# Optimization experiments

Hardware: AMD Instinct MI355X
Metric: run time of the kernel (lower is better)

Reference implementation:

```python
import jax, jax.numpy as jnp
import numpy as np
import math

B, C, H, W = 8, 64, 256, 256
E, NH = 256, 8
HD = E // NH  # 32


def get_coords(h, w):
    xx, yy = jnp.meshgrid(jnp.arange(h, dtype=jnp.float32), jnp.arange(w, dtype=jnp.float32), indexing='ij')
    return jnp.stack((xx.reshape(-1), yy.reshape(-1)), axis=-1)  # [N, 2]


def setup_inputs() -> dict:
    key = jax.random.key(0)
    ks = jax.random.split(key, 12)
    def xavier(k, shape):
        fan_out, fan_in = shape
        a = math.sqrt(6.0 / (fan_in + fan_out))
        return jax.random.uniform(k, shape, jnp.float32, -a, a)
    x = jax.random.normal(ks[0], (B, C, H, W), jnp.float32)
    z = jax.random.normal(ks[1], (B, C), jnp.float32)
    pos = jax.random.uniform(ks[2], (B, NH, 2), jnp.float32) * (H - 1)
    Wq = xavier(ks[3], (E, C)); bq = jnp.zeros((E,), jnp.float32)
    Wk = xavier(ks[4], (E, C)); bk = jnp.zeros((E,), jnp.float32)
    Wv = xavier(ks[5], (E, C)); bv = jnp.zeros((E,), jnp.float32)
    Wp = xavier(ks[6], (HD, 2)); bp = jax.random.uniform(ks[7], (HD,), jnp.float32, -1.0, 1.0) / math.sqrt(2.0)
    return {"x": x, "z": z, "pos": pos, "Wq": Wq, "bq": bq, "Wk": Wk, "bk": bk,
            "Wv": Wv, "bv": bv, "Wp": Wp, "bp": bp}


def reference(x, z, pos, Wq, bq, Wk, bk, Wv, bv, Wp, bp):
    b, c, h, w = x.shape
    n = h * w
    x_flat = x.reshape(b, c, n).transpose(0, 2, 1)          # [B, N, C]
    pos_grid = get_coords(h, w)                              # [N, 2]
    q = (z @ Wq.T + bq).reshape(b, NH, HD)                   # [B, H, hd]
    k = (x_flat @ Wk.T + bk).reshape(b, n, NH, HD)           # [B, N, H, hd]
    # relative-position modulation of keys
    rel = pos_grid[None, :, None, :] - pos[:, None, :, :]    # [B, N, H, 2]
    qxk = rel @ Wp.T + bp                                    # [B, N, H, hd]
    k = k * qxk
    v = x_flat @ Wv.T + bv                                   # [B, N, E]
    attn_logits = jnp.einsum('bhc,bnhc->bnh', q, k) / math.sqrt(HD)
    attention = jax.nn.softmax(attn_logits, axis=1)          # softmax over N
    pos_out = jnp.einsum('bnh,nx->bhx', attention, pos_grid) # [B, H, 2]
    values = jnp.einsum('bnh,bnc->bhc', attention, v)        # [B, H, E]
    return (values, pos_out)
```

## Files before the change

kernel.cpp:

```cpp
#include <hip/hip_runtime.h>

#define NN    65536
#define NSUB  256
#define NBLK  (NN/NSUB)
#define WPAD  260

#define OFF_W   0
#define SZ_W    (8*64*24)
#define OFF_CJ  (OFF_W + SZ_W)
#define SZ_CJ   (8*24)
#define OFF_PM  (OFF_CJ + SZ_CJ)
#define SZ_P    (8*NBLK*8)
#define OFF_PL  (OFF_PM + SZ_P)
#define OFF_PSP (OFF_PL + SZ_P)
#define OFF_PSX (OFF_PSP + 2*SZ_P)

#define SMEM1_FLOATS (64*WPAD + 8*NSUB + 128)
#define SMEM1_BYTES  (SMEM1_FLOATS*4)

__global__ __launch_bounds__(64) void prep_kernel(
    const float* __restrict__ z,  const float* __restrict__ Wq, const float* __restrict__ bq,
    const float* __restrict__ Wk, const float* __restrict__ bk,
    const float* __restrict__ Wp, const float* __restrict__ bp,
    float* __restrict__ Weff, float* __restrict__ Cj)
{
  const int h = blockIdx.x, b = blockIdx.y, t = threadIdx.x;
  __shared__ float q[32];
  if (t < 32) {
    const int e = h*32 + t;
    float a = bq[e];
    const float* zr = z + b*64;
    const float* wr = Wq + e*64;
    #pragma unroll 8
    for (int c = 0; c < 64; ++c) a += zr[c]*wr[c];
    q[t] = a;
  }
  __syncthreads();
  {
    const int c = t;
    float w0 = 0.f, w1 = 0.f, w2 = 0.f;
    #pragma unroll 4
    for (int hd = 0; hd < 32; ++hd) {
      const float qk = q[hd] * Wk[(h*32+hd)*64 + c];
      w0 += qk * bp[hd];
      w1 += qk * Wp[hd*2+0];
      w2 += qk * Wp[hd*2+1];
    }
    float* o = Weff + (b*64 + c)*24 + h*3;
    o[0] = w0; o[1] = w1; o[2] = w2;
  }
  if (t < 3) {
    float s = 0.f;
    for (int hd = 0; hd < 32; ++hd) {
      const float m = (t == 0) ? bp[hd] : Wp[hd*2 + (t-1)];
      s += q[hd] * m * bk[h*32+hd];
    }
    Cj[b*24 + h*3 + t] = s;
  }
}

__global__ __launch_bounds__(256) void main_kernel(
    const float* __restrict__ x, const float* __restrict__ pos,
    const float* __restrict__ Weff, const float* __restrict__ Cj,
    float* __restrict__ Pm, float* __restrict__ Pl,
    float* __restrict__ Psp, float* __restrict__ Psx)
{
  extern __shared__ float sm[];
  float* xs  = sm;
  float* ps  = sm + 64*WPAD;
  float* red = ps + 8*NSUB;
  const int t   = threadIdx.x;
  const int blk = blockIdx.x;
  const int b   = blockIdx.y;
  const int n0  = blk * NSUB;

  {
    const float* xb = x + (size_t)b*64*NN + n0;
    #pragma unroll
    for (int r = 0; r < 16; ++r) {
      const int f  = t + r*256;
      const int c  = f >> 6;
      const int p4 = (f & 63) << 2;
      const float4 v = *(const float4*)(xb + (size_t)c*NN + p4);
      *(float4*)(xs + c*WPAD + p4) = v;
    }
  }

  float cj[24];
  #pragma unroll
  for (int k = 0; k < 24; ++k) cj[k] = Cj[b*24 + k];
  float px[8], py[8];
  #pragma unroll
  for (int h = 0; h < 8; ++h) { px[h] = pos[(b*8+h)*2 + 0]; py[h] = pos[(b*8+h)*2 + 1]; }

  __syncthreads();

  float acc[24];
  #pragma unroll
  for (int k = 0; k < 24; ++k) acc[k] = cj[k];
  const float* wb = Weff + b*64*24;
  for (int c = 0; c < 64; ++c) {
    const float xv = xs[c*WPAD + t];
    const float* wr = wb + c*24;
    #pragma unroll
    for (int k = 0; k < 24; ++k) acc[k] += wr[k]*xv;
  }
  const int   n  = n0 + t;
  const float gx = (float)(n >> 8);
  const float gy = (float)(n & 255);
  float lg[8];
  #pragma unroll
  for (int h = 0; h < 8; ++h) {
    const float rx = gx - px[h];
    const float ry = gy - py[h];
    lg[h] = (acc[h*3+0] + rx*acc[h*3+1] + ry*acc[h*3+2]) * 0.17677669529663687f;
  }

  float mh[8];
  #pragma unroll
  for (int h = 0; h < 8; ++h) {
    float m = lg[h];
    #pragma unroll
    for (int off = 32; off >= 1; off >>= 1) m = fmaxf(m, __shfl_xor(m, off, 64));
    mh[h] = m;
  }
  const int wid = t >> 6, lid = t & 63;
  if (lid == 0) {
    #pragma unroll
    for (int h = 0; h < 8; ++h) red[h*4 + wid] = mh[h];
  }
  __syncthreads();

  float p[8], trip[24];
  #pragma unroll
  for (int h = 0; h < 8; ++h) {
    const float M = fmaxf(fmaxf(red[h*4+0], red[h*4+1]), fmaxf(red[h*4+2], red[h*4+3]));
    mh[h] = M;
    p[h]  = __expf(lg[h] - M);
    trip[h*3+0] = p[h];
    trip[h*3+1] = p[h]*gx;
    trip[h*3+2] = p[h]*gy;
  }
  #pragma unroll
  for (int k = 0; k < 24; ++k) {
    float s = trip[k];
    #pragma unroll
    for (int off = 32; off >= 1; off >>= 1) s += __shfl_xor(s, off, 64);
    trip[k] = s;
  }
  if (lid == 0) {
    #pragma unroll
    for (int k = 0; k < 24; ++k) red[32 + k*4 + wid] = trip[k];
  }
  #pragma unroll
  for (int h = 0; h < 8; ++h) ps[h*NSUB + t] = p[h];
  __syncthreads();

  if (t < 8) {
    const int h = t;
    const int base = (b*NBLK + blk)*8 + h;
    Pm[base] = mh[h];
    Pl[base] = red[32+(h*3+0)*4+0] + red[32+(h*3+0)*4+1] + red[32+(h*3+0)*4+2] + red[32+(h*3+0)*4+3];
    Psp[base*2+0] = red[32+(h*3+1)*4+0] + red[32+(h*3+1)*4+1] + red[32+(h*3+1)*4+2] + red[32+(h*3+1)*4+3];
    Psp[base*2+1] = red[32+(h*3+2)*4+0] + red[32+(h*3+2)*4+1] + red[32+(h*3+2)*4+2] + red[32+(h*3+2)*4+3];
  }

  {
    const int c  = t & 63;
    const int h0 = t >> 6;
    const float* xr  = xs + c*WPAD;
    const float* pr0 = ps + h0*NSUB;
    const float* pr1 = ps + (h0+4)*NSUB;
    float a0 = 0.f, a1 = 0.f;
    #pragma unroll 4
    for (int nn = 0; nn < NSUB; nn += 4) {
      const float4 xv = *(const float4*)(xr  + nn);
      const float4 q0 = *(const float4*)(pr0 + nn);
      const float4 q1 = *(const float4*)(pr1 + nn);
      a0 += xv.x*q0.x + xv.y*q0.y + xv.z*q0.z + xv.w*q0.w;
      a1 += xv.x*q1.x + xv.y*q1.y + xv.z*q1.z + xv.w*q1.w;
    }
    const int pb = (b*NBLK + blk)*8;
    Psx[(pb + h0    )*64 + c] = a0;
    Psx[(pb + h0 + 4)*64 + c] = a1;
  }
}

__global__ __launch_bounds__(256) void finish_kernel(
    const float* __restrict__ Pm, const float* __restrict__ Pl,
    const float* __restrict__ Psp, const float* __restrict__ Psx,
    const float* __restrict__ Wv, const float* __restrict__ bv,
    float* __restrict__ out)
{
  const int h = blockIdx.x, b = blockIdx.y, t = threadIdx.x;
  __shared__ float al[256];
  __shared__ float red[16];
  __shared__ float sxl[256];
  __shared__ float SXs[64];
  const int wid = t >> 6, lid = t & 63;
  const int pbase = (b*NBLK + t)*8 + h;

  const float m_t = Pm[pbase];
  float mm = m_t;
  #pragma unroll
  for (int off = 32; off >= 1; off >>= 1) mm = fmaxf(mm, __shfl_xor(mm, off, 64));
  if (lid == 0) red[wid] = mm;
  __syncthreads();
  const float M = fmaxf(fmaxf(red[0], red[1]), fmaxf(red[2], red[3]));
  const float a = __expf(m_t - M);
  al[t] = a;
  float lt  = Pl[pbase] * a;
  float sxt = Psp[pbase*2+0] * a;
  float syt = Psp[pbase*2+1] * a;
  #pragma unroll
  for (int off = 32; off >= 1; off >>= 1) {
    lt  += __shfl_xor(lt,  off, 64);
    sxt += __shfl_xor(sxt, off, 64);
    syt += __shfl_xor(syt, off, 64);
  }
  if (lid == 0) { red[4+wid] = lt; red[8+wid] = sxt; red[12+wid] = syt; }
  __syncthreads();
  const float L = red[4]+red[5]+red[6]+red[7];
  const float invL = 1.0f / L;

  const int c = t & 63, g = t >> 6;
  float acc = 0.f;
  for (int k = 0; k < 64; ++k) {
    const int blk = g*64 + k;
    acc += Psx[((b*NBLK + blk)*8 + h)*64 + c] * al[blk];
  }
  sxl[g*64 + c] = acc;
  __syncthreads();
  if (t < 64) SXs[t] = (sxl[t] + sxl[64+t] + sxl[128+t] + sxl[192+t]) * invL;
  __syncthreads();

  float v = bv[t];
  const float* wvr = Wv + t*64;
  #pragma unroll 8
  for (int c2 = 0; c2 < 64; ++c2) v += wvr[c2] * SXs[c2];
  out[(b*8+h)*256 + t] = v;

  if (t == 0) {
    const float SPx = red[8]+red[9]+red[10]+red[11];
    const float SPy = red[12]+red[13]+red[14]+red[15];
    out[16384 + (b*8+h)*2 + 0] = SPx * invL;
    out[16384 + (b*8+h)*2 + 1] = SPy * invL;
  }
}

extern "C" void kernel_launch(void* const* d_in, const int* in_sizes, int n_in,
                              void* d_out, int out_size, void* d_ws, size_t ws_size,
                              hipStream_t stream)
{
  const float* x   = (const float*)d_in[0];
  const float* z   = (const float*)d_in[1];
  const float* pos = (const float*)d_in[2];
  const float* Wq  = (const float*)d_in[3];
  const float* bq  = (const float*)d_in[4];
  const float* Wk  = (const float*)d_in[5];
  const float* bk  = (const float*)d_in[6];
  const float* Wv  = (const float*)d_in[7];
  const float* bv  = (const float*)d_in[8];
  const float* Wp  = (const float*)d_in[9];
  const float* bp  = (const float*)d_in[10];
  float* out = (float*)d_out;
  float* ws  = (float*)d_ws;

  float* Weff = ws + OFF_W;
  float* Cj   = ws + OFF_CJ;
  float* Pm   = ws + OFF_PM;
  float* Pl   = ws + OFF_PL;
  float* Psp  = ws + OFF_PSP;
  float* Psx  = ws + OFF_PSX;

  (void)hipFuncSetAttribute((const void*)main_kernel,
                            hipFuncAttributeMaxDynamicSharedMemorySize, SMEM1_BYTES);

  prep_kernel  <<<dim3(8,8),    64,  0,           stream>>>(z, Wq, bq, Wk, bk, Wp, bp, Weff, Cj);
  main_kernel  <<<dim3(NBLK,8), 256, SMEM1_BYTES, stream>>>(x, pos, Weff, Cj, Pm, Pl, Psp, Psx);
  finish_kernel<<<dim3(8,8),    256, 0,           stream>>>(Pm, Pl, Psp, Psx, Wv, bv, out);
}
```

Measured before the change: 281.4 us.

## Stage Weff in LDS, restructure softmax partial sums and widen finish kernel

Measured after the change: 264.7 us. 5.9% less time.

```diff
diff --git a/kernel.cpp b/kernel.cpp
--- a/kernel.cpp
+++ b/kernel.cpp
@@ -15,7 +15,7 @@
 #define OFF_PSP (OFF_PL + SZ_P)
 #define OFF_PSX (OFF_PSP + 2*SZ_P)
 
-#define SMEM1_FLOATS (64*WPAD + 8*NSUB + 128)
+#define SMEM1_FLOATS (64*WPAD + 8*256 + 1536 + 64)
 #define SMEM1_BYTES  (SMEM1_FLOATS*4)
 
 __global__ __launch_bounds__(64) void prep_kernel(
@@ -67,12 +67,14 @@
 {
   extern __shared__ float sm[];
   float* xs  = sm;
-  float* ps  = sm + 64*WPAD;
-  float* red = ps + 8*NSUB;
+  float* ps  = xs + 64*WPAD;
+  float* wsw = ps + 8*256;
+  float* red = wsw + 1536;
   const int t   = threadIdx.x;
   const int blk = blockIdx.x;
   const int b   = blockIdx.y;
   const int n0  = blk * NSUB;
+  const int wid = t >> 6, lid = t & 63;
 
   {
     const float* xb = x + (size_t)b*64*NN + n0;
@@ -84,37 +86,42 @@
       const float4 v = *(const float4*)(xb + (size_t)c*NN + p4);
       *(float4*)(xs + c*WPAD + p4) = v;
     }
+    const float* wsrc = Weff + b*1536;
+    #pragma unroll
+    for (int r = 0; r < 6; ++r) wsw[t + r*256] = wsrc[t + r*256];
   }
 
   float cj[24];
   #pragma unroll
   for (int k = 0; k < 24; ++k) cj[k] = Cj[b*24 + k];
-  float px[8], py[8];
-  #pragma unroll
-  for (int h = 0; h < 8; ++h) { px[h] = pos[(b*8+h)*2 + 0]; py[h] = pos[(b*8+h)*2 + 1]; }
-
-  __syncthreads();
-
-  float acc[24];
-  #pragma unroll
-  for (int k = 0; k < 24; ++k) acc[k] = cj[k];
-  const float* wb = Weff + b*64*24;
+  float rxh[8], py[8];
+  #pragma unroll
+  for (int h = 0; h < 8; ++h) {
+    rxh[h] = (float)blk - pos[(b*8+h)*2 + 0];
+    py[h]  = pos[(b*8+h)*2 + 1];
+  }
+
+  __syncthreads();
+
+  float2 acc2[12];
+  #pragma unroll
+  for (int j = 0; j < 12; ++j) acc2[j] = make_float2(cj[2*j], cj[2*j+1]);
+  #pragma unroll 2
   for (int c = 0; c < 64; ++c) {
     const float xv = xs[c*WPAD + t];
-    const float* wr = wb + c*24;
-    #pragma unroll
-    for (int k = 0; k < 24; ++k) acc[k] += wr[k]*xv;
-  }
-  const int   n  = n0 + t;
-  const float gx = (float)(n >> 8);
-  const float gy = (float)(n & 255);
+    const float2* wr = (const float2*)(wsw + c*24);
+    #pragma unroll
+    for (int j = 0; j < 12; ++j) {
+      acc2[j].x += wr[j].x * xv;
+      acc2[j].y += wr[j].y * xv;
+    }
+  }
+  const float* acc = (const float*)acc2;
+  const float tyf = (float)t;
   float lg[8];
   #pragma unroll
-  for (int h = 0; h < 8; ++h) {
-    const float rx = gx - px[h];
-    const float ry = gy - py[h];
-    lg[h] = (acc[h*3+0] + rx*acc[h*3+1] + ry*acc[h*3+2]) * 0.17677669529663687f;
-  }
+  for (int h = 0; h < 8; ++h)
+    lg[h] = (acc[h*3+0] + rxh[h]*acc[h*3+1] + (tyf - py[h])*acc[h*3+2]) * 0.17677669529663687f;
 
   float mh[8];
   #pragma unroll
@@ -124,69 +131,81 @@
     for (int off = 32; off >= 1; off >>= 1) m = fmaxf(m, __shfl_xor(m, off, 64));
     mh[h] = m;
   }
-  const int wid = t >> 6, lid = t & 63;
   if (lid == 0) {
     #pragma unroll
     for (int h = 0; h < 8; ++h) red[h*4 + wid] = mh[h];
   }
   __syncthreads();
 
-  float p[8], trip[24];
   #pragma unroll
   for (int h = 0; h < 8; ++h) {
     const float M = fmaxf(fmaxf(red[h*4+0], red[h*4+1]), fmaxf(red[h*4+2], red[h*4+3]));
     mh[h] = M;
-    p[h]  = __expf(lg[h] - M);
-    trip[h*3+0] = p[h];
-    trip[h*3+1] = p[h]*gx;
-    trip[h*3+2] = p[h]*gy;
-  }
-  #pragma unroll
-  for (int k = 0; k < 24; ++k) {
-    float s = trip[k];
-    #pragma unroll
-    for (int off = 32; off >= 1; off >>= 1) s += __shfl_xor(s, off, 64);
-    trip[k] = s;
-  }
-  if (lid == 0) {
-    #pragma unroll
-    for (int k = 0; k < 24; ++k) red[32 + k*4 + wid] = trip[k];
-  }
-  #pragma unroll
-  for (int h = 0; h < 8; ++h) ps[h*NSUB + t] = p[h];
-  __syncthreads();
-
-  if (t < 8) {
-    const int h = t;
-    const int base = (b*NBLK + blk)*8 + h;
-    Pm[base] = mh[h];
-    Pl[base] = red[32+(h*3+0)*4+0] + red[32+(h*3+0)*4+1] + red[32+(h*3+0)*4+2] + red[32+(h*3+0)*4+3];
-    Psp[base*2+0] = red[32+(h*3+1)*4+0] + red[32+(h*3+1)*4+1] + red[32+(h*3+1)*4+2] + red[32+(h*3+1)*4+3];
-    Psp[base*2+1] = red[32+(h*3+2)*4+0] + red[32+(h*3+2)*4+1] + red[32+(h*3+2)*4+2] + red[32+(h*3+2)*4+3];
-  }
-
-  {
-    const int c  = t & 63;
-    const int h0 = t >> 6;
-    const float* xr  = xs + c*WPAD;
-    const float* pr0 = ps + h0*NSUB;
-    const float* pr1 = ps + (h0+4)*NSUB;
-    float a0 = 0.f, a1 = 0.f;
-    #pragma unroll 4
-    for (int nn = 0; nn < NSUB; nn += 4) {
-      const float4 xv = *(const float4*)(xr  + nn);
-      const float4 q0 = *(const float4*)(pr0 + nn);
-      const float4 q1 = *(const float4*)(pr1 + nn);
-      a0 += xv.x*q0.x + xv.y*q0.y + xv.z*q0.z + xv.w*q0.w;
-      a1 += xv.x*q1.x + xv.y*q1.y + xv.z*q1.z + xv.w*q1.w;
-    }
+    ps[h*256 + t] = __expf(lg[h] - M);
+  }
+  __syncthreads();
+
+  {
+    const int h0 = wid*2;
+    const float4 pa = *(const float4*)(ps + h0*256 + 4*lid);
+    const float4 pb = *(const float4*)(ps + (h0+1)*256 + 4*lid);
+    const float j0 = (float)(4*lid);
+    float s0a = pa.x + pa.y + pa.z + pa.w;
+    float s1a = pa.x*j0 + pa.y*(j0+1.f) + pa.z*(j0+2.f) + pa.w*(j0+3.f);
+    float s0b = pb.x + pb.y + pb.z + pb.w;
+    float s1b = pb.x*j0 + pb.y*(j0+1.f) + pb.z*(j0+2.f) + pb.w*(j0+3.f);
+    #pragma unroll
+    for (int off = 32; off >= 1; off >>= 1) {
+      s0a += __shfl_xor(s0a, off, 64);
+      s1a += __shfl_xor(s1a, off, 64);
+      s0b += __shfl_xor(s0b, off, 64);
+      s1b += __shfl_xor(s1b, off, 64);
+    }
+    if (lid == 0) {
+      const int base = (b*NBLK + blk)*8;
+      const float blkf = (float)blk;
+      Pm[base+h0]   = mh[h0];   Pl[base+h0]   = s0a;
+      Psp[(base+h0)*2+0]   = blkf*s0a;  Psp[(base+h0)*2+1]   = s1a;
+      Pm[base+h0+1] = mh[h0+1]; Pl[base+h0+1] = s0b;
+      Psp[(base+h0+1)*2+0] = blkf*s0b;  Psp[(base+h0+1)*2+1] = s1b;
+    }
+  }
+
+  float aB[8];
+  #pragma unroll
+  for (int h = 0; h < 8; ++h) aB[h] = 0.f;
+  {
+    const int nq = wid*64;
+    const float* xr = xs + lid*WPAD + nq;
+    #pragma unroll 2
+    for (int j = 0; j < 16; ++j) {
+      const float4 xv = *(const float4*)(xr + 4*j);
+      #pragma unroll
+      for (int h = 0; h < 8; ++h) {
+        const float4 pv = *(const float4*)(ps + h*256 + nq + 4*j);
+        aB[h] += pv.x*xv.x + pv.y*xv.y + pv.z*xv.z + pv.w*xv.w;
+      }
+    }
+  }
+  __syncthreads();
+  {
+    float* part = sm;
+    #pragma unroll
+    for (int h = 0; h < 8; ++h) part[(wid*8 + h)*64 + lid] = aB[h];
+  }
+  __syncthreads();
+  {
     const int pb = (b*NBLK + blk)*8;
-    Psx[(pb + h0    )*64 + c] = a0;
-    Psx[(pb + h0 + 4)*64 + c] = a1;
+    #pragma unroll
+    for (int r = 0; r < 2; ++r) {
+      const int idx = t + 256*r;
+      const float s = sm[idx] + sm[512+idx] + sm[1024+idx] + sm[1536+idx];
+      Psx[(size_t)pb*64 + idx] = s;
+    }
   }
 }
 
-__global__ __launch_bounds__(256) void finish_kernel(
+__global__ __launch_bounds__(1024) void finish_kernel(
     const float* __restrict__ Pm, const float* __restrict__ Pl,
     const float* __restrict__ Psp, const float* __restrict__ Psx,
     const float* __restrict__ Wv, const float* __restrict__ bv,
@@ -194,55 +213,69 @@
 {
   const int h = blockIdx.x, b = blockIdx.y, t = threadIdx.x;
   __shared__ float al[256];
-  __shared__ float red[16];
-  __shared__ float sxl[256];
+  __shared__ float redm[32];
+  __shared__ float sxl[1024];
   __shared__ float SXs[64];
   const int wid = t >> 6, lid = t & 63;
-  const int pbase = (b*NBLK + t)*8 + h;
-
-  const float m_t = Pm[pbase];
-  float mm = m_t;
-  #pragma unroll
-  for (int off = 32; off >= 1; off >>= 1) mm = fmaxf(mm, __shfl_xor(mm, off, 64));
-  if (lid == 0) red[wid] = mm;
-  __syncthreads();
-  const float M = fmaxf(fmaxf(red[0], red[1]), fmaxf(red[2], red[3]));
-  const float a = __expf(m_t - M);
-  al[t] = a;
-  float lt  = Pl[pbase] * a;
-  float sxt = Psp[pbase*2+0] * a;
-  float syt = Psp[pbase*2+1] * a;
-  #pragma unroll
-  for (int off = 32; off >= 1; off >>= 1) {
-    lt  += __shfl_xor(lt,  off, 64);
-    sxt += __shfl_xor(sxt, off, 64);
-    syt += __shfl_xor(syt, off, 64);
-  }
-  if (lid == 0) { red[4+wid] = lt; red[8+wid] = sxt; red[12+wid] = syt; }
-  __syncthreads();
-  const float L = red[4]+red[5]+red[6]+red[7];
+
+  float m_t = 0.f;
+  if (t < 256) {
+    m_t = Pm[(b*NBLK + t)*8 + h];
+    float mm = m_t;
+    #pragma unroll
+    for (int off = 32; off >= 1; off >>= 1) mm = fmaxf(mm, __shfl_xor(mm, off, 64));
+    if (lid == 0) redm[wid] = mm;
+  }
+  __syncthreads();
+  const float M = fmaxf(fmaxf(redm[0], redm[1]), fmaxf(redm[2], redm[3]));
+  if (t < 256) {
+    const int pbase = (b*NBLK + t)*8 + h;
+    const float a = __expf(m_t - M);
+    al[t] = a;
+    float lt  = Pl[pbase] * a;
+    float sxt = Psp[pbase*2+0] * a;
+    float syt = Psp[pbase*2+1] * a;
+    #pragma unroll
+    for (int off = 32; off >= 1; off >>= 1) {
+      lt  += __shfl_xor(lt,  off, 64);
+      sxt += __shfl_xor(sxt, off, 64);
+      syt += __shfl_xor(syt, off, 64);
+    }
+    if (lid == 0) { redm[4+wid] = lt; redm[8+wid] = sxt; redm[12+wid] = syt; }
+  }
+  __syncthreads();
+  const float L = redm[4]+redm[5]+redm[6]+redm[7];
   const float invL = 1.0f / L;
 
-  const int c = t & 63, g = t >> 6;
-  float acc = 0.f;
-  for (int k = 0; k < 64; ++k) {
-    const int blk = g*64 + k;
-    acc += Psx[((b*NBLK + blk)*8 + h)*64 + c] * al[blk];
-  }
-  sxl[g*64 + c] = acc;
-  __syncthreads();
-  if (t < 64) SXs[t] = (sxl[t] + sxl[64+t] + sxl[128+t] + sxl[192+t]) * invL;
-  __syncthreads();
-
-  float v = bv[t];
-  const float* wvr = Wv + t*64;
-  #pragma unroll 8
-  for (int c2 = 0; c2 < 64; ++c2) v += wvr[c2] * SXs[c2];
-  out[(b*8+h)*256 + t] = v;
-
+  {
+    const int c = lid, g = wid;
+    float acc = 0.f;
+    #pragma unroll
+    for (int k = 0; k < 16; ++k) {
+      const int blk = g*16 + k;
+      acc += Psx[((size_t)(b*NBLK + blk)*8 + h)*64 + c] * al[blk];
+    }
+    sxl[g*64 + c] = acc;
+  }
+  __syncthreads();
+  if (t < 64) {
+    float s = 0.f;
+    #pragma unroll
+    for (int g = 0; g < 16; ++g) s += sxl[g*64 + t];
+    SXs[t] = s * invL;
+  }
+  __syncthreads();
+
+  if (t < 256) {
+    float v = bv[t];
+    const float* wvr = Wv + t*64;
+    #pragma unroll 8
+    for (int c2 = 0; c2 < 64; ++c2) v += wvr[c2] * SXs[c2];
+    out[(b*8+h)*256 + t] = v;
+  }
   if (t == 0) {
-    const float SPx = red[8]+red[9]+red[10]+red[11];
-    const float SPy = red[12]+red[13]+red[14]+red[15];
+    const float SPx = redm[8]+redm[9]+redm[10]+redm[11];
+    const float SPy = redm[12]+redm[13]+redm[14]+redm[15];
     out[16384 + (b*8+h)*2 + 0] = SPx * invL;
     out[16384 + (b*8+h)*2 + 1] = SPy * invL;
   }
@@ -276,7 +309,7 @@
   (void)hipFuncSetAttribute((const void*)main_kernel,
                             hipFuncAttributeMaxDynamicSharedMemorySize, SMEM1_BYTES);
 
-  prep_kernel  <<<dim3(8,8),    64,  0,           stream>>>(z, Wq, bq, Wk, bk, Wp, bp, Weff, Cj);
-  main_kernel  <<<dim3(NBLK,8), 256, SMEM1_BYTES, stream>>>(x, pos, Weff, Cj, Pm, Pl, Psp, Psx);
-  finish_kernel<<<dim3(8,8),    256, 0,           stream>>>(Pm, Pl, Psp, Psx, Wv, bv, out);
+  prep_kernel  <<<dim3(8,8),    64,   0,           stream>>>(z, Wq, bq, Wk, bk, Wp, bp, Weff, Cj);
+  main_kernel  <<<dim3(NBLK,8), 256,  SMEM1_BYTES, stream>>>(x, pos, Weff, Cj, Pm, Pl, Psp, Psx);
+  finish_kernel<<<dim3(8,8),    1024, 0,           stream>>>(Pm, Pl, Psp, Psx, Wv, bv, out);
 }
```
